# Kernel tuning notes

Hardware: AMD Instinct MI355X
Metric: run time of the kernel (lower is better)

Reference implementation:

```python
import jax, jax.numpy as jnp
import numpy as np

N, C, K = 100000, 64, 27
EPS = 1e-5


def setup_inputs() -> dict:
    key = jax.random.key(0)
    ks = jax.random.split(key, 8)
    feats = jax.random.normal(ks[0], (N, C), dtype=jnp.float32)
    W1 = jax.random.normal(ks[1], (K, C, C), dtype=jnp.float32) * (1.0 / np.sqrt(K * C))
    W2 = jax.random.normal(ks[2], (K, C, C), dtype=jnp.float32) * (1.0 / np.sqrt(K * C))
    gamma1 = jnp.ones((C,), dtype=jnp.float32)
    beta1 = jnp.zeros((C,), dtype=jnp.float32)
    gamma2 = jnp.ones((C,), dtype=jnp.float32)
    beta2 = jnp.zeros((C,), dtype=jnp.float32)
    nbr_idx1 = jax.random.randint(ks[3], (K, N), 0, N, dtype=jnp.int32)
    nbr_idx2 = jax.random.randint(ks[4], (K, N), 0, N, dtype=jnp.int32)
    nbr_mask1 = (jax.random.uniform(ks[5], (K, N)) < 0.7).astype(jnp.float32)
    nbr_mask2 = (jax.random.uniform(ks[6], (K, N)) < 0.7).astype(jnp.float32)
    return {"feats": feats, "W1": W1, "gamma1": gamma1, "beta1": beta1,
            "W2": W2, "gamma2": gamma2, "beta2": beta2,
            "nbr_idx1": nbr_idx1, "nbr_mask1": nbr_mask1,
            "nbr_idx2": nbr_idx2, "nbr_mask2": nbr_mask2}


def sparse_conv(f, idx, mask, W):
    # gather per kernel offset: [K, N, C], mask out missing neighbors
    g = f[idx] * mask[..., None]
    # per-offset GEMM and accumulate over offsets -> [N, C_out]
    return jnp.einsum('knc,kcd->nd', g, W)


def batch_norm(x, gamma, beta):
    # MinkowskiBatchNorm (training): stats over all N points, per channel
    mean = jnp.mean(x, axis=0)
    var = jnp.mean(jnp.square(x - mean), axis=0)
    return (x - mean) * jax.lax.rsqrt(var + EPS) * gamma + beta


def reference(feats, W1, gamma1, beta1, W2, gamma2, beta2,
              nbr_idx1, nbr_mask1, nbr_idx2, nbr_mask2):
    out = sparse_conv(feats, nbr_idx1, nbr_mask1, W1)
    out = jax.nn.relu(batch_norm(out, gamma1, beta1))
    out = sparse_conv(out, nbr_idx2, nbr_mask2, W2)
    out = batch_norm(out, gamma2, beta2)
    out = out + feats          # identity residual (stride=1, no downsample)
    return jax.nn.relu(out)
```

## Files before the change

kernel.cpp:

```cpp
#include <hip/hip_runtime.h>
#include <hip/hip_bf16.h>
#include <stdint.h>
#include <stddef.h>

#define N_PTS 100000
#define KOFF 27

typedef __attribute__((ext_vector_type(8))) __bf16 bf16x8;
typedef __attribute__((ext_vector_type(4))) float f32x4;
typedef __attribute__((ext_vector_type(8))) unsigned short ushort8;

__device__ inline unsigned short f2bf(float f) {
  union { float f; unsigned u; } x; x.f = f;
  unsigned r = x.u + 0x7fffu + ((x.u >> 16) & 1u);
  return (unsigned short)(r >> 16);
}
__device__ inline float bf2f(unsigned short b) {
  union { unsigned u; float f; } x; x.u = ((unsigned)b) << 16;
  return x.f;
}

__global__ __launch_bounds__(256) void prep_kernel(const float* __restrict__ feats,
                                                   const float* __restrict__ W1,
                                                   const float* __restrict__ W2,
                                                   unsigned short* __restrict__ featsb,
                                                   unsigned short* __restrict__ f2b,
                                                   unsigned short* __restrict__ wf1,
                                                   unsigned short* __restrict__ wf2,
                                                   float* __restrict__ stats) {
  __shared__ float sW[4096];
  int t = threadIdx.x;
  if (blockIdx.x < 54) {
    int which = blockIdx.x & 1;
    int k = blockIdx.x >> 1;
    const float* W = (which ? W2 : W1) + (size_t)k * 4096;
    unsigned short* wf = (which ? wf2 : wf1) + (size_t)k * 4096;
#pragma unroll
    for (int i = 0; i < 4; ++i)
      ((float4*)sW)[t + 256 * i] = ((const float4*)W)[t + 256 * i];
    __syncthreads();
#pragma unroll
    for (int i = 0; i < 16; ++i) {
      int o = i * 256 + t;
      int j = o & 7, l = (o >> 3) & 63, nt = (o >> 9) & 3, kk = (o >> 11) & 1;
      int c = kk * 32 + ((l >> 4) << 3) + j;
      int d = nt * 16 + (l & 15);
      wf[o] = f2bf(sW[c * 64 + d]);
    }
    return;
  }
  int fb = blockIdx.x - 54;
  int NB = gridDim.x - 54;
  const int NF4 = N_PTS * 16;
  for (int i = fb * 256 + t; i < NF4; i += NB * 256) {
    float4 v = ((const float4*)feats)[i];
    ushort4 o;
    o.x = f2bf(v.x); o.y = f2bf(v.y); o.z = f2bf(v.z); o.w = f2bf(v.w);
    ((ushort4*)featsb)[i] = o;
  }
  if (fb == 0) {
    if (t < 256) stats[t] = 0.f;
    uint4 z = make_uint4(0u, 0u, 0u, 0u);
    if (t < 8)            ((uint4*)(featsb + (size_t)N_PTS * 64))[t] = z;
    if (t >= 8 && t < 16) ((uint4*)(f2b    + (size_t)N_PTS * 64))[t - 8] = z;
  }
}

#define MFMA16(a, b, c) __builtin_amdgcn_mfma_f32_16x16x32_bf16(__builtin_bit_cast(bf16x8, a), __builtin_bit_cast(bf16x8, b), c, 0, 0, 0)

#define STEP(kcur, Ac0, Ac1, An0, An1, iN, mN, iF, mF)                          \
  {                                                                             \
    const size_t kn = (size_t)((kcur) + 1) * 8192;                              \
    S0 = *(const uint4*)(wfB + kn + t16);                                       \
    S1 = *(const uint4*)(wfB + kn + 4096 + t16);                                \
    {                                                                           \
      int gie = (mN != 0.f) ? iN : N_PTS;                                       \
      const char* rp = (const char*)fin + (size_t)gie * 128 + g16;              \
      An0 = *(const uint4*)rp; An1 = *(const uint4*)(rp + 64);                  \
    }                                                                           \
    {                                                                           \
      int kf = ((kcur) + 2 <= 26) ? (kcur) + 2 : 26;                            \
      iF = idxp[(size_t)kf * N_PTS];                                            \
      float mt = mp[(size_t)kf * N_PTS]; mF = valid ? mt : 0.f;                 \
    }                                                                           \
    {                                                                           \
      const uint4* bL = (const uint4*)sB[cur];                                  \
      uint4 b0 = bL[lane],       b1 = bL[64 + lane];                            \
      uint4 b2 = bL[128 + lane], b3 = bL[192 + lane];                           \
      uint4 b4 = bL[256 + lane], b5 = bL[320 + lane];                           \
      uint4 b6 = bL[384 + lane], b7 = bL[448 + lane];                           \
      a0 = MFMA16(Ac0, b0, a0); a1 = MFMA16(Ac0, b1, a1);                       \
      a2 = MFMA16(Ac0, b2, a2); a3 = MFMA16(Ac0, b3, a3);                       \
      a0 = MFMA16(Ac1, b4, a0); a1 = MFMA16(Ac1, b5, a1);                       \
      a2 = MFMA16(Ac1, b6, a2); a3 = MFMA16(Ac1, b7, a3);                       \
    }                                                                           \
    {                                                                           \
      uint4* wL = (uint4*)sB[cur ^ 1];                                          \
      wL[t] = S0; wL[t + 256] = S1;                                             \
    }                                                                           \
    __syncthreads();                                                            \
    cur ^= 1;                                                                   \
  }

__global__ __launch_bounds__(256, 6) void conv_kernel(
    const unsigned short* __restrict__ fin,
    const unsigned short* __restrict__ wf,
    const int* __restrict__ idx,
    const float* __restrict__ mask,
    unsigned short* __restrict__ yout,
    float* __restrict__ gsum,
    float* __restrict__ gsq)
{
  __shared__ __align__(16) unsigned char sB[2][8192];
  __shared__ float s_sum[64], s_sq[64];

  int t    = threadIdx.x;
  int lane = t & 63;
  int wid  = t >> 6;
  int m    = lane & 15;
  int g    = lane >> 4;
  int g16  = g * 16;
  size_t t16 = (size_t)t * 16;
  int nw   = blockIdx.x * 64 + wid * 16;
  int n    = nw + m;
  bool valid = n < N_PTS;
  int nc   = valid ? n : 0;

  const int*   idxp = idx + nc;
  const float* mp   = mask + nc;
  const char*  wfB  = (const char*)wf;

  if (t < 64) { s_sum[t] = 0.f; s_sq[t] = 0.f; }

  f32x4 a0, a1, a2, a3;
#pragma unroll
  for (int r = 0; r < 4; ++r) { a0[r] = 0.f; a1[r] = 0.f; a2[r] = 0.f; a3[r] = 0.f; }

  uint4 Aa0, Aa1, Ba0, Ba1, S0, S1;
  int iA, iB; float mA, mB;
  int cur = 0;

  iA = idxp[0]; { float mt = mp[0]; mA = valid ? mt : 0.f; }
  S0 = *(const uint4*)(wfB + t16);
  S1 = *(const uint4*)(wfB + 4096 + t16);
  {
    int gie = (mA != 0.f) ? iA : N_PTS;
    const char* rp = (const char*)fin + (size_t)gie * 128 + g16;
    Aa0 = *(const uint4*)rp; Aa1 = *(const uint4*)(rp + 64);
  }
  iB = idxp[N_PTS]; { float mt = mp[N_PTS]; mB = valid ? mt : 0.f; }
  {
    uint4* wL = (uint4*)sB[0];
    wL[t] = S0; wL[t + 256] = S1;
  }
  __syncthreads();

  for (int kk = 0; kk < 13; ++kk) {
    int k = 2 * kk;
    STEP(k,     Aa0, Aa1,  Ba0, Ba1,  iB, mB,  iA, mA);
    STEP(k + 1, Ba0, Ba1,  Aa0, Aa1,  iA, mA,  iB, mB);
  }

  {
    const uint4* bL = (const uint4*)sB[cur];
    uint4 b0 = bL[lane],       b1 = bL[64 + lane];
    uint4 b2 = bL[128 + lane], b3 = bL[192 + lane];
    uint4 b4 = bL[256 + lane], b5 = bL[320 + lane];
    uint4 b6 = bL[384 + lane], b7 = bL[448 + lane];
    a0 = MFMA16(Aa0, b0, a0); a1 = MFMA16(Aa0, b1, a1);
    a2 = MFMA16(Aa0, b2, a2); a3 = MFMA16(Aa0, b3, a3);
    a0 = MFMA16(Aa1, b4, a0); a1 = MFMA16(Aa1, b5, a1);
    a2 = MFMA16(Aa1, b6, a2); a3 = MFMA16(Aa1, b7, a3);
  }

  float s0 = 0.f, q0 = 0.f, s1 = 0.f, q1 = 0.f;
  float s2 = 0.f, q2 = 0.f, s3 = 0.f, q3 = 0.f;
#pragma unroll
  for (int r = 0; r < 4; ++r) {
    int row = nw + g * 4 + r;
    float v0 = a0[r]; s0 += v0; q0 += v0 * v0;
    float v1 = a1[r]; s1 += v1; q1 += v1 * v1;
    float v2 = a2[r]; s2 += v2; q2 += v2 * v2;
    float v3 = a3[r]; s3 += v3; q3 += v3 * v3;
    if (row < N_PTS) {
      unsigned short* yr = yout + (size_t)row * 64;
      yr[m]      = f2bf(v0);
      yr[16 + m] = f2bf(v1);
      yr[32 + m] = f2bf(v2);
      yr[48 + m] = f2bf(v3);
    }
  }
  atomicAdd(&s_sum[m],      s0); atomicAdd(&s_sq[m],      q0);
  atomicAdd(&s_sum[16 + m], s1); atomicAdd(&s_sq[16 + m], q1);
  atomicAdd(&s_sum[32 + m], s2); atomicAdd(&s_sq[32 + m], q2);
  atomicAdd(&s_sum[48 + m], s3); atomicAdd(&s_sq[48 + m], q3);
  __syncthreads();
  if (t < 64) {
    atomicAdd(&gsum[t], s_sum[t]);
    atomicAdd(&gsq[t],  s_sq[t]);
  }
}

__global__ void bn1_kernel(const unsigned short* __restrict__ y,
                           const float* __restrict__ sum,
                           const float* __restrict__ sq,
                           const float* __restrict__ gamma,
                           const float* __restrict__ beta,
                           unsigned short* __restrict__ outb) {
  __shared__ float s_scale[64], s_shift[64];
  if (threadIdx.x < 64) {
    int c = threadIdx.x;
    float mean = sum[c] * (1.f / N_PTS);
    float var  = sq[c] * (1.f / N_PTS) - mean * mean;
    float inv  = rsqrtf(var + 1e-5f);
    float sc   = gamma[c] * inv;
    s_scale[c] = sc;
    s_shift[c] = beta[c] - mean * sc;
  }
  __syncthreads();
  int tid = blockIdx.x * blockDim.x + threadIdx.x;
  int stride = gridDim.x * blockDim.x;
  const int NT = N_PTS * 8;
  for (int i = tid; i < NT; i += stride) {
    ushort8 v = ((const ushort8*)y)[i];
    int c = (i * 8) & 63;
    ushort8 o;
#pragma unroll
    for (int j = 0; j < 8; ++j) {
      float f = bf2f(v[j]);
      o[j] = f2bf(fmaxf(f * s_scale[c + j] + s_shift[c + j], 0.f));
    }
    ((ushort8*)outb)[i] = o;
  }
}

__global__ void bn2_kernel(const unsigned short* __restrict__ y,
                           const float* __restrict__ sum,
                           const float* __restrict__ sq,
                           const float* __restrict__ gamma,
                           const float* __restrict__ beta,
                           const float* __restrict__ feats,
                           float* __restrict__ out) {
  __shared__ float s_scale[64], s_shift[64];
  if (threadIdx.x < 64) {
    int c = threadIdx.x;
    float mean = sum[c] * (1.f / N_PTS);
    float var  = sq[c] * (1.f / N_PTS) - mean * mean;
    float inv  = rsqrtf(var + 1e-5f);
    float sc   = gamma[c] * inv;
    s_scale[c] = sc;
    s_shift[c] = beta[c] - mean * sc;
  }
  __syncthreads();
  int tid = blockIdx.x * blockDim.x + threadIdx.x;
  int stride = gridDim.x * blockDim.x;
  const int NT = N_PTS * 8;
  for (int i = tid; i < NT; i += stride) {
    ushort8 v = ((const ushort8*)y)[i];
    float4 f0 = ((const float4*)feats)[i * 2];
    float4 f1 = ((const float4*)feats)[i * 2 + 1];
    int c = (i * 8) & 63;
    float4 o0, o1;
    o0.x = fmaxf(bf2f(v[0]) * s_scale[c]     + s_shift[c]     + f0.x, 0.f);
    o0.y = fmaxf(bf2f(v[1]) * s_scale[c + 1] + s_shift[c + 1] + f0.y, 0.f);
    o0.z = fmaxf(bf2f(v[2]) * s_scale[c + 2] + s_shift[c + 2] + f0.z, 0.f);
    o0.w = fmaxf(bf2f(v[3]) * s_scale[c + 3] + s_shift[c + 3] + f0.w, 0.f);
    o1.x = fmaxf(bf2f(v[4]) * s_scale[c + 4] + s_shift[c + 4] + f1.x, 0.f);
    o1.y = fmaxf(bf2f(v[5]) * s_scale[c + 5] + s_shift[c + 5] + f1.y, 0.f);
    o1.z = fmaxf(bf2f(v[6]) * s_scale[c + 6] + s_shift[c + 6] + f1.z, 0.f);
    o1.w = fmaxf(bf2f(v[7]) * s_scale[c + 7] + s_shift[c + 7] + f1.w, 0.f);
    ((float4*)out)[i * 2]     = o0;
    ((float4*)out)[i * 2 + 1] = o1;
  }
}

extern "C" void kernel_launch(void* const* d_in, const int* in_sizes, int n_in,
                              void* d_out, int out_size, void* d_ws, size_t ws_size,
                              hipStream_t stream) {
  const float* feats  = (const float*)d_in[0];
  const float* W1     = (const float*)d_in[1];
  const float* gamma1 = (const float*)d_in[2];
  const float* beta1  = (const float*)d_in[3];
  const float* W2     = (const float*)d_in[4];
  const float* gamma2 = (const float*)d_in[5];
  const float* beta2  = (const float*)d_in[6];
  const int*   idx1   = (const int*)d_in[7];
  const float* mask1  = (const float*)d_in[8];
  const int*   idx2   = (const int*)d_in[9];
  const float* mask2  = (const float*)d_in[10];
  float* out = (float*)d_out;

  char* ws = (char*)d_ws;
  unsigned short* featsb = (unsigned short*)(ws + 0);
  unsigned short* wf1    = (unsigned short*)(ws + 12800768);
  unsigned short* wf2    = (unsigned short*)(ws + 13021952);
  float*          stats  = (float*)(ws + 13243136);
  unsigned short* f2b    = (unsigned short*)(ws + 13244160);

  float* sum1 = stats;       float* sq1 = stats + 64;
  float* sum2 = stats + 128; float* sq2 = stats + 192;

  unsigned short* y1 = (unsigned short*)d_out;
  unsigned short* y2 = featsb;

  prep_kernel<<<54 + 640, 256, 0, stream>>>(feats, W1, W2, featsb, f2b, wf1, wf2, stats);

  const int CONV_GRID = (N_PTS + 63) / 64;
  conv_kernel<<<CONV_GRID, 256, 0, stream>>>(featsb, wf1, idx1, mask1, y1, sum1, sq1);
  bn1_kernel<<<1024, 256, 0, stream>>>(y1, sum1, sq1, gamma1, beta1, f2b);
  conv_kernel<<<CONV_GRID, 256, 0, stream>>>(f2b, wf2, idx2, mask2, y2, sum2, sq2);
  bn2_kernel<<<1024, 256, 0, stream>>>(y2, sum2, sq2, gamma2, beta2, feats, out);
}
```

Baseline: 310.3 us.

## Fuse BN1+ReLU into second conv gather and split channels into two halves

Removes the standalone bn1 kernel by applying BN1 scale/shift and ReLU on the fly to the gathered neighbor rows inside the second conv, masking afterwards. Features and intermediates are stored as separate 32-channel low/high halves, and the conv runs two passes over the 27 offsets, one per half. The point of the halves is a smaller per-pass gather footprint and half the LDS weight buffer. In exchange, the idx/mask arrays are read twice, the BN transform is recomputed once per neighbor (27x per point), and the occupancy hint drops from 6 to 4.

```diff
diff --git a/kernel.cpp b/kernel.cpp
--- a/kernel.cpp
+++ b/kernel.cpp
@@ -23,8 +23,10 @@
 __global__ __launch_bounds__(256) void prep_kernel(const float* __restrict__ feats,
                                                    const float* __restrict__ W1,
                                                    const float* __restrict__ W2,
-                                                   unsigned short* __restrict__ featsb,
-                                                   unsigned short* __restrict__ f2b,
+                                                   unsigned short* __restrict__ flo,
+                                                   unsigned short* __restrict__ fhi,
+                                                   unsigned short* __restrict__ ylo,
+                                                   unsigned short* __restrict__ yhi,
                                                    unsigned short* __restrict__ wf1,
                                                    unsigned short* __restrict__ wf2,
                                                    float* __restrict__ stats) {
@@ -34,7 +36,7 @@
     int which = blockIdx.x & 1;
     int k = blockIdx.x >> 1;
     const float* W = (which ? W2 : W1) + (size_t)k * 4096;
-    unsigned short* wf = (which ? wf2 : wf1) + (size_t)k * 4096;
+    unsigned short* wf = (which ? wf2 : wf1);
 #pragma unroll
     for (int i = 0; i < 4; ++i)
       ((float4*)sW)[t + 256 * i] = ((const float4*)W)[t + 256 * i];
@@ -45,7 +47,7 @@
       int j = o & 7, l = (o >> 3) & 63, nt = (o >> 9) & 3, kk = (o >> 11) & 1;
       int c = kk * 32 + ((l >> 4) << 3) + j;
       int d = nt * 16 + (l & 15);
-      wf[o] = f2bf(sW[c * 64 + d]);
+      wf[kk * 55296 + k * 2048 + nt * 512 + l * 8 + j] = f2bf(sW[c * 64 + d]);
     }
     return;
   }
@@ -54,29 +56,43 @@
   const int NF4 = N_PTS * 16;
   for (int i = fb * 256 + t; i < NF4; i += NB * 256) {
     float4 v = ((const float4*)feats)[i];
-    ushort4 o;
-    o.x = f2bf(v.x); o.y = f2bf(v.y); o.z = f2bf(v.z); o.w = f2bf(v.w);
-    ((ushort4*)featsb)[i] = o;
+    int n = i >> 4, q = i & 15;
+    ushort4 o4;
+    o4.x = f2bf(v.x); o4.y = f2bf(v.y); o4.z = f2bf(v.z); o4.w = f2bf(v.w);
+    if (q < 8) ((ushort4*)(flo + (size_t)n * 32))[q]     = o4;
+    else       ((ushort4*)(fhi + (size_t)n * 32))[q - 8] = o4;
   }
   if (fb == 0) {
     if (t < 256) stats[t] = 0.f;
     uint4 z = make_uint4(0u, 0u, 0u, 0u);
-    if (t < 8)            ((uint4*)(featsb + (size_t)N_PTS * 64))[t] = z;
-    if (t >= 8 && t < 16) ((uint4*)(f2b    + (size_t)N_PTS * 64))[t - 8] = z;
+    if (t < 4)                ((uint4*)(flo + (size_t)N_PTS * 32))[t]      = z;
+    else if (t < 8)           ((uint4*)(fhi + (size_t)N_PTS * 32))[t - 4]  = z;
+    else if (t < 12)          ((uint4*)(ylo + (size_t)N_PTS * 32))[t - 8]  = z;
+    else if (t < 16)          ((uint4*)(yhi + (size_t)N_PTS * 32))[t - 12] = z;
   }
 }
 
 #define MFMA16(a, b, c) __builtin_amdgcn_mfma_f32_16x16x32_bf16(__builtin_bit_cast(bf16x8, a), __builtin_bit_cast(bf16x8, b), c, 0, 0, 0)
 
-#define STEP(kcur, Ac0, Ac1, An0, An1, iN, mN, iF, mF)                          \
+#define XFORM(dst, Asrc, mC)                                                    \
   {                                                                             \
-    const size_t kn = (size_t)((kcur) + 1) * 8192;                              \
-    S0 = *(const uint4*)(wfB + kn + t16);                                       \
-    S1 = *(const uint4*)(wfB + kn + 4096 + t16);                                \
+    ushort8 v_ = __builtin_bit_cast(ushort8, Asrc);                             \
+    ushort8 o_;                                                                 \
+    _Pragma("unroll")                                                           \
+    for (int e_ = 0; e_ < 8; ++e_) {                                            \
+      float f_ = bf2f(v_[e_]);                                                  \
+      o_[e_] = f2bf(fmaxf(f_ * sc8[e_] + sh8[e_], 0.f) * (mC));                 \
+    }                                                                           \
+    dst = __builtin_bit_cast(uint4, o_);                                        \
+  }
+
+#define STEP(kcur, Ac, An, iN, mN, iF, mF)                                      \
+  {                                                                             \
+    float mC = mF;                                                              \
+    S0 = *(const uint4*)(wfP + (size_t)((kcur) + 1) * 2048 + t8);               \
     {                                                                           \
       int gie = (mN != 0.f) ? iN : N_PTS;                                       \
-      const char* rp = (const char*)fin + (size_t)gie * 128 + g16;              \
-      An0 = *(const uint4*)rp; An1 = *(const uint4*)(rp + 64);                  \
+      An = *(const uint4*)((const char*)finP + (size_t)gie * 64 + g16);         \
     }                                                                           \
     {                                                                           \
       int kf = ((kcur) + 2 <= 26) ? (kcur) + 2 : 26;                            \
@@ -87,31 +103,32 @@
       const uint4* bL = (const uint4*)sB[cur];                                  \
       uint4 b0 = bL[lane],       b1 = bL[64 + lane];                            \
       uint4 b2 = bL[128 + lane], b3 = bL[192 + lane];                           \
-      uint4 b4 = bL[256 + lane], b5 = bL[320 + lane];                           \
-      uint4 b6 = bL[384 + lane], b7 = bL[448 + lane];                           \
-      a0 = MFMA16(Ac0, b0, a0); a1 = MFMA16(Ac0, b1, a1);                       \
-      a2 = MFMA16(Ac0, b2, a2); a3 = MFMA16(Ac0, b3, a3);                       \
-      a0 = MFMA16(Ac1, b4, a0); a1 = MFMA16(Ac1, b5, a1);                       \
-      a2 = MFMA16(Ac1, b6, a2); a3 = MFMA16(Ac1, b7, a3);                       \
+      uint4 Ax;                                                                 \
+      if (dobn) { XFORM(Ax, Ac, mC); } else { Ax = Ac; }                        \
+      a0 = MFMA16(Ax, b0, a0); a1 = MFMA16(Ax, b1, a1);                         \
+      a2 = MFMA16(Ax, b2, a2); a3 = MFMA16(Ax, b3, a3);                         \
     }                                                                           \
-    {                                                                           \
-      uint4* wL = (uint4*)sB[cur ^ 1];                                          \
-      wL[t] = S0; wL[t + 256] = S1;                                             \
-    }                                                                           \
+    ((uint4*)sB[cur ^ 1])[t] = S0;                                              \
     __syncthreads();                                                            \
     cur ^= 1;                                                                   \
   }
 
-__global__ __launch_bounds__(256, 6) void conv_kernel(
-    const unsigned short* __restrict__ fin,
+__global__ __launch_bounds__(256, 4) void conv_kernel(
+    const unsigned short* __restrict__ flo,
+    const unsigned short* __restrict__ fhi,
     const unsigned short* __restrict__ wf,
     const int* __restrict__ idx,
     const float* __restrict__ mask,
-    unsigned short* __restrict__ yout,
+    const float* __restrict__ bnsum,
+    const float* __restrict__ bnsq,
+    const float* __restrict__ gamma,
+    const float* __restrict__ beta,
+    unsigned short* __restrict__ ylo,
+    unsigned short* __restrict__ yhi,
     float* __restrict__ gsum,
     float* __restrict__ gsq)
 {
-  __shared__ __align__(16) unsigned char sB[2][8192];
+  __shared__ __align__(16) unsigned char sB[2][4096];
   __shared__ float s_sum[64], s_sq[64];
 
   int t    = threadIdx.x;
@@ -120,15 +137,15 @@
   int m    = lane & 15;
   int g    = lane >> 4;
   int g16  = g * 16;
-  size_t t16 = (size_t)t * 16;
+  size_t t8 = (size_t)t * 8;
   int nw   = blockIdx.x * 64 + wid * 16;
   int n    = nw + m;
   bool valid = n < N_PTS;
   int nc   = valid ? n : 0;
+  bool dobn = (bnsum != nullptr);
 
   const int*   idxp = idx + nc;
   const float* mp   = mask + nc;
-  const char*  wfB  = (const char*)wf;
 
   if (t < 64) { s_sum[t] = 0.f; s_sq[t] = 0.f; }
 
@@ -136,41 +153,56 @@
 #pragma unroll
   for (int r = 0; r < 4; ++r) { a0[r] = 0.f; a1[r] = 0.f; a2[r] = 0.f; a3[r] = 0.f; }
 
-  uint4 Aa0, Aa1, Ba0, Ba1, S0, S1;
-  int iA, iB; float mA, mB;
-  int cur = 0;
-
-  iA = idxp[0]; { float mt = mp[0]; mA = valid ? mt : 0.f; }
-  S0 = *(const uint4*)(wfB + t16);
-  S1 = *(const uint4*)(wfB + 4096 + t16);
-  {
-    int gie = (mA != 0.f) ? iA : N_PTS;
-    const char* rp = (const char*)fin + (size_t)gie * 128 + g16;
-    Aa0 = *(const uint4*)rp; Aa1 = *(const uint4*)(rp + 64);
-  }
-  iB = idxp[N_PTS]; { float mt = mp[N_PTS]; mB = valid ? mt : 0.f; }
-  {
-    uint4* wL = (uint4*)sB[0];
-    wL[t] = S0; wL[t + 256] = S1;
-  }
-  __syncthreads();
-
-  for (int kk = 0; kk < 13; ++kk) {
-    int k = 2 * kk;
-    STEP(k,     Aa0, Aa1,  Ba0, Ba1,  iB, mB,  iA, mA);
-    STEP(k + 1, Ba0, Ba1,  Aa0, Aa1,  iA, mA,  iB, mB);
-  }
-
-  {
-    const uint4* bL = (const uint4*)sB[cur];
-    uint4 b0 = bL[lane],       b1 = bL[64 + lane];
-    uint4 b2 = bL[128 + lane], b3 = bL[192 + lane];
-    uint4 b4 = bL[256 + lane], b5 = bL[320 + lane];
-    uint4 b6 = bL[384 + lane], b7 = bL[448 + lane];
-    a0 = MFMA16(Aa0, b0, a0); a1 = MFMA16(Aa0, b1, a1);
-    a2 = MFMA16(Aa0, b2, a2); a3 = MFMA16(Aa0, b3, a3);
-    a0 = MFMA16(Aa1, b4, a0); a1 = MFMA16(Aa1, b5, a1);
-    a2 = MFMA16(Aa1, b6, a2); a3 = MFMA16(Aa1, b7, a3);
+  for (int p = 0; p < 2; ++p) {
+    const unsigned short* finP = p ? fhi : flo;
+    const unsigned short* wfP  = wf + (size_t)p * 55296;
+
+    float sc8[8], sh8[8];
+    if (dobn) {
+#pragma unroll
+      for (int e = 0; e < 8; ++e) {
+        int c = p * 32 + g * 8 + e;
+        float mean = bnsum[c] * (1.f / N_PTS);
+        float var  = bnsq[c] * (1.f / N_PTS) - mean * mean;
+        float inv  = rsqrtf(var + 1e-5f);
+        sc8[e] = gamma[c] * inv;
+        sh8[e] = beta[c] - mean * sc8[e];
+      }
+    } else {
+#pragma unroll
+      for (int e = 0; e < 8; ++e) { sc8[e] = 1.f; sh8[e] = 0.f; }
+    }
+
+    uint4 Aa, Ab, S0;
+    int iA, iB; float mA, mB;
+    int cur = 0;
+    iA = idxp[0]; { float mt = mp[0]; mA = valid ? mt : 0.f; }
+    S0 = *(const uint4*)(wfP + t8);
+    {
+      int gie = (mA != 0.f) ? iA : N_PTS;
+      Aa = *(const uint4*)((const char*)finP + (size_t)gie * 64 + g16);
+    }
+    iB = idxp[N_PTS]; { float mt = mp[N_PTS]; mB = valid ? mt : 0.f; }
+    ((uint4*)sB[0])[t] = S0;
+    __syncthreads();
+
+    for (int kk = 0; kk < 13; ++kk) {
+      int k = 2 * kk;
+      STEP(k,     Aa, Ab, iB, mB, iA, mA);
+      STEP(k + 1, Ab, Aa, iA, mA, iB, mB);
+    }
+
+    {
+      const uint4* bL = (const uint4*)sB[cur];
+      uint4 b0 = bL[lane],       b1 = bL[64 + lane];
+      uint4 b2 = bL[128 + lane], b3 = bL[192 + lane];
+      uint4 Ax;
+      float mC = mA;
+      if (dobn) { XFORM(Ax, Aa, mC); } else { Ax = Aa; }
+      a0 = MFMA16(Ax, b0, a0); a1 = MFMA16(Ax, b1, a1);
+      a2 = MFMA16(Ax, b2, a2); a3 = MFMA16(Ax, b3, a3);
+    }
+    __syncthreads();
   }
 
   float s0 = 0.f, q0 = 0.f, s1 = 0.f, q1 = 0.f;
@@ -183,11 +215,12 @@
     float v2 = a2[r]; s2 += v2; q2 += v2 * v2;
     float v3 = a3[r]; s3 += v3; q3 += v3 * v3;
     if (row < N_PTS) {
-      unsigned short* yr = yout + (size_t)row * 64;
-      yr[m]      = f2bf(v0);
-      yr[16 + m] = f2bf(v1);
-      yr[32 + m] = f2bf(v2);
-      yr[48 + m] = f2bf(v3);
+      unsigned short* yl = ylo + (size_t)row * 32;
+      unsigned short* yh = yhi + (size_t)row * 32;
+      yl[m]      = f2bf(v0);
+      yl[16 + m] = f2bf(v1);
+      yh[m]      = f2bf(v2);
+      yh[16 + m] = f2bf(v3);
     }
   }
   atomicAdd(&s_sum[m],      s0); atomicAdd(&s_sq[m],      q0);
@@ -201,40 +234,8 @@
   }
 }
 
-__global__ void bn1_kernel(const unsigned short* __restrict__ y,
-                           const float* __restrict__ sum,
-                           const float* __restrict__ sq,
-                           const float* __restrict__ gamma,
-                           const float* __restrict__ beta,
-                           unsigned short* __restrict__ outb) {
-  __shared__ float s_scale[64], s_shift[64];
-  if (threadIdx.x < 64) {
-    int c = threadIdx.x;
-    float mean = sum[c] * (1.f / N_PTS);
-    float var  = sq[c] * (1.f / N_PTS) - mean * mean;
-    float inv  = rsqrtf(var + 1e-5f);
-    float sc   = gamma[c] * inv;
-    s_scale[c] = sc;
-    s_shift[c] = beta[c] - mean * sc;
-  }
-  __syncthreads();
-  int tid = blockIdx.x * blockDim.x + threadIdx.x;
-  int stride = gridDim.x * blockDim.x;
-  const int NT = N_PTS * 8;
-  for (int i = tid; i < NT; i += stride) {
-    ushort8 v = ((const ushort8*)y)[i];
-    int c = (i * 8) & 63;
-    ushort8 o;
-#pragma unroll
-    for (int j = 0; j < 8; ++j) {
-      float f = bf2f(v[j]);
-      o[j] = f2bf(fmaxf(f * s_scale[c + j] + s_shift[c + j], 0.f));
-    }
-    ((ushort8*)outb)[i] = o;
-  }
-}
-
-__global__ void bn2_kernel(const unsigned short* __restrict__ y,
+__global__ void bn2_kernel(const unsigned short* __restrict__ y2lo,
+                           const unsigned short* __restrict__ y2hi,
                            const float* __restrict__ sum,
                            const float* __restrict__ sq,
                            const float* __restrict__ gamma,
@@ -254,23 +255,39 @@
   __syncthreads();
   int tid = blockIdx.x * blockDim.x + threadIdx.x;
   int stride = gridDim.x * blockDim.x;
-  const int NT = N_PTS * 8;
+  const int NT = N_PTS * 4;
   for (int i = tid; i < NT; i += stride) {
-    ushort8 v = ((const ushort8*)y)[i];
-    float4 f0 = ((const float4*)feats)[i * 2];
-    float4 f1 = ((const float4*)feats)[i * 2 + 1];
-    int c = (i * 8) & 63;
-    float4 o0, o1;
-    o0.x = fmaxf(bf2f(v[0]) * s_scale[c]     + s_shift[c]     + f0.x, 0.f);
-    o0.y = fmaxf(bf2f(v[1]) * s_scale[c + 1] + s_shift[c + 1] + f0.y, 0.f);
-    o0.z = fmaxf(bf2f(v[2]) * s_scale[c + 2] + s_shift[c + 2] + f0.z, 0.f);
-    o0.w = fmaxf(bf2f(v[3]) * s_scale[c + 3] + s_shift[c + 3] + f0.w, 0.f);
-    o1.x = fmaxf(bf2f(v[4]) * s_scale[c + 4] + s_shift[c + 4] + f1.x, 0.f);
-    o1.y = fmaxf(bf2f(v[5]) * s_scale[c + 5] + s_shift[c + 5] + f1.y, 0.f);
-    o1.z = fmaxf(bf2f(v[6]) * s_scale[c + 6] + s_shift[c + 6] + f1.z, 0.f);
-    o1.w = fmaxf(bf2f(v[7]) * s_scale[c + 7] + s_shift[c + 7] + f1.w, 0.f);
-    ((float4*)out)[i * 2]     = o0;
-    ((float4*)out)[i * 2 + 1] = o1;
+    int n = i >> 2, q = i & 3, c0 = q * 8;
+    ushort8 lo = ((const ushort8*)y2lo)[(size_t)n * 4 + q];
+    ushort8 hi = ((const ushort8*)y2hi)[(size_t)n * 4 + q];
+    const float* fp = feats + (size_t)n * 64 + c0;
+    float* op = out + (size_t)n * 64 + c0;
+    float4 f0 = ((const float4*)fp)[0];
+    float4 f1 = ((const float4*)fp)[1];
+    float4 f2 = ((const float4*)(fp + 32))[0];
+    float4 f3 = ((const float4*)(fp + 32))[1];
+    float4 o0, o1, o2, o3;
+    o0.x = fmaxf(bf2f(lo[0]) * s_scale[c0]     + s_shift[c0]     + f0.x, 0.f);
+    o0.y = fmaxf(bf2f(lo[1]) * s_scale[c0 + 1] + s_shift[c0 + 1] + f0.y, 0.f);
+    o0.z = fmaxf(bf2f(lo[2]) * s_scale[c0 + 2] + s_shift[c0 + 2] + f0.z, 0.f);
+    o0.w = fmaxf(bf2f(lo[3]) * s_scale[c0 + 3] + s_shift[c0 + 3] + f0.w, 0.f);
+    o1.x = fmaxf(bf2f(lo[4]) * s_scale[c0 + 4] + s_shift[c0 + 4] + f1.x, 0.f);
+    o1.y = fmaxf(bf2f(lo[5]) * s_scale[c0 + 5] + s_shift[c0 + 5] + f1.y, 0.f);
+    o1.z = fmaxf(bf2f(lo[6]) * s_scale[c0 + 6] + s_shift[c0 + 6] + f1.z, 0.f);
+    o1.w = fmaxf(bf2f(lo[7]) * s_scale[c0 + 7] + s_shift[c0 + 7] + f1.w, 0.f);
+    int ch = 32 + c0;
+    o2.x = fmaxf(bf2f(hi[0]) * s_scale[ch]     + s_shift[ch]     + f2.x, 0.f);
+    o2.y = fmaxf(bf2f(hi[1]) * s_scale[ch + 1] + s_shift[ch + 1] + f2.y, 0.f);
+    o2.z = fmaxf(bf2f(hi[2]) * s_scale[ch + 2] + s_shift[ch + 2] + f2.z, 0.f);
+    o2.w = fmaxf(bf2f(hi[3]) * s_scale[ch + 3] + s_shift[ch + 3] + f2.w, 0.f);
+    o3.x = fmaxf(bf2f(hi[4]) * s_scale[ch + 4] + s_shift[ch + 4] + f3.x, 0.f);
+    o3.y = fmaxf(bf2f(hi[5]) * s_scale[ch + 5] + s_shift[ch + 5] + f3.y, 0.f);
+    o3.z = fmaxf(bf2f(hi[6]) * s_scale[ch + 6] + s_shift[ch + 6] + f3.z, 0.f);
+    o3.w = fmaxf(bf2f(hi[7]) * s_scale[ch + 7] + s_shift[ch + 7] + f3.w, 0.f);
+    ((float4*)op)[0] = o0;
+    ((float4*)op)[1] = o1;
+    ((float4*)(op + 32))[0] = o2;
+    ((float4*)(op + 32))[1] = o3;
   }
 }
 
@@ -291,23 +308,25 @@
   float* out = (float*)d_out;
 
   char* ws = (char*)d_ws;
-  unsigned short* featsb = (unsigned short*)(ws + 0);
-  unsigned short* wf1    = (unsigned short*)(ws + 12800768);
-  unsigned short* wf2    = (unsigned short*)(ws + 13021952);
-  float*          stats  = (float*)(ws + 13243136);
-  unsigned short* f2b    = (unsigned short*)(ws + 13244160);
+  unsigned short* flo   = (unsigned short*)(ws + 0);
+  unsigned short* fhi   = (unsigned short*)(ws + 6400128);
+  unsigned short* ylo   = (unsigned short*)(ws + 12800256);
+  unsigned short* yhi   = (unsigned short*)(ws + 19200384);
+  unsigned short* wf1   = (unsigned short*)(ws + 25600512);
+  unsigned short* wf2   = (unsigned short*)(ws + 25821696);
+  float*          stats = (float*)(ws + 26042880);
 
   float* sum1 = stats;       float* sq1 = stats + 64;
   float* sum2 = stats + 128; float* sq2 = stats + 192;
 
-  unsigned short* y1 = (unsigned short*)d_out;
-  unsigned short* y2 = featsb;
-
-  prep_kernel<<<54 + 640, 256, 0, stream>>>(feats, W1, W2, featsb, f2b, wf1, wf2, stats);
+  prep_kernel<<<54 + 640, 256, 0, stream>>>(feats, W1, W2, flo, fhi, ylo, yhi, wf1, wf2, stats);
 
   const int CONV_GRID = (N_PTS + 63) / 64;
-  conv_kernel<<<CONV_GRID, 256, 0, stream>>>(featsb, wf1, idx1, mask1, y1, sum1, sq1);
-  bn1_kernel<<<1024, 256, 0, stream>>>(y1, sum1, sq1, gamma1, beta1, f2b);
-  conv_kernel<<<CONV_GRID, 256, 0, stream>>>(f2b, wf2, idx2, mask2, y2, sum2, sq2);
-  bn2_kernel<<<1024, 256, 0, stream>>>(y2, sum2, sq2, gamma2, beta2, feats, out);
-}
+  conv_kernel<<<CONV_GRID, 256, 0, stream>>>(flo, fhi, wf1, idx1, mask1,
+                                             nullptr, nullptr, nullptr, nullptr,
+                                             ylo, yhi, sum1, sq1);
+  conv_kernel<<<CONV_GRID, 256, 0, stream>>>(ylo, yhi, wf2, idx2, mask2,
+                                             sum1, sq1, gamma1, beta1,
+                                             flo, fhi, sum2, sq2);
+  bn2_kernel<<<1024, 256, 0, stream>>>(flo, fhi, sum2, sq2, gamma2, beta2, feats, out);
+}
```

Measured after the change: 330.7 us. 6.6% more time.
